# Optimization experiments

Hardware: AMD Instinct MI355X
Metric: run time of the kernel (lower is better)

The kernel has to match this reference:

```python
import jax, jax.numpy as jnp
import numpy as np

BOUND = 1.0 - 1e-16  # margin = 1e-16 (note: rounds to 1.0 in float32, same as torch float32)


def _lpc_to_par(a):
    # Backward Levinson-Durbin: LPC (K, a_1..a_M) -> PARCOR (K, k_1..k_M)
    K, c = a[..., :1], a[..., 1:]
    M = c.shape[-1]
    idx = jnp.arange(M)

    def step(c, m):  # m goes M, M-1, ..., 1
        k = jnp.take(c, m - 1, axis=-1)  # k_m = a_m^(m), shape (B,)
        # paired[j] = a_{m-1-j}^(m) for j=0..m-2 (i.e. a_{m-i} for i=1..m-1)
        paired = jnp.roll(jnp.flip(c, -1), -(M - m + 1), axis=-1)
        c2 = (c - k[..., None] * paired) / (1.0 - k[..., None] ** 2)
        c = jnp.where(idx < m - 1, c2, c)
        return c, k

    _, ks = jax.lax.scan(step, c, jnp.arange(M, 0, -1))
    k1 = jnp.flip(jnp.moveaxis(ks, 0, -1), -1)  # reorder to k_1..k_M, shape (B, M)
    return jnp.concatenate([K, k1], axis=-1)


def _par_to_lpc(k):
    # Forward Levinson-Durbin: PARCOR (K, k_1..k_M) -> LPC (K, a_1..a_M)
    K, kk = k[..., :1], k[..., 1:]
    M = kk.shape[-1]
    idx = jnp.arange(M)
    c0 = jnp.zeros_like(kk)

    def step(c, mk):  # m goes 1..M
        m, km = mk
        paired = jnp.roll(jnp.flip(c, -1), -(M - m + 1), axis=-1)
        c2 = c + km[..., None] * paired
        c = jnp.where(idx < m - 1, c2, c)
        c = jnp.where(idx == m - 1, km[..., None], c)
        return c, None

    ks = jnp.moveaxis(kk, -1, 0)  # (M, B)
    cM, _ = jax.lax.scan(step, c0, (jnp.arange(1, M + 1), ks))
    return jnp.concatenate([K, cM], axis=-1)


def setup_inputs() -> dict:
    key = jax.random.key(0)
    B, M = 2_000_000, 24
    # scale down so the backward Levinson recursion is well-conditioned
    a = 0.05 * jax.random.normal(key, (B, M + 1), dtype=jnp.float32)
    return {"a": a}


def reference(a):
    k = _lpc_to_par(a)
    K, k1 = k[..., :1], k[..., 1:]
    # warn_type='ignore': no side effect; just clip to stability bound
    k1 = jnp.clip(k1, -BOUND, BOUND)
    k2 = jnp.concatenate([K, k1], axis=-1)
    return _par_to_lpc(k2)
```

## Files before the change

### kernel.cpp

```cpp
#include <hip/hip_runtime.h>

#define MM 24
#define ROW_LEN (MM + 1)
#define RPB 256
#define FPB (RPB * ROW_LEN)
#define V4PB (FPB / 4)

__global__ __launch_bounds__(RPB)
void lpc_stab_kernel(const float* __restrict__ a, float* __restrict__ out, int B) {
    __shared__ float lds[FPB];

    const long long total4 = ((long long)B * ROW_LEN) >> 2;
    const long long base4  = (long long)blockIdx.x * V4PB;
    const float4* a4 = (const float4*)a;
    float4*       o4 = (float4*)out;
    float4*       l4 = (float4*)lds;

    #pragma unroll
    for (int it = 0; it < 7; ++it) {
        int li = it * RPB + threadIdx.x;
        if (li < V4PB) {
            long long g = base4 + li;
            if (g < total4) l4[li] = a4[g];
        }
    }
    __syncthreads();

    const int row = blockIdx.x * RPB + threadIdx.x;
    if (row < B) {
        float* p = lds + threadIdx.x * ROW_LEN;
        float K = p[0];
        float c[MM], k[MM];
        #pragma unroll
        for (int j = 0; j < MM; ++j) c[j] = p[j + 1];

        #pragma unroll
        for (int m = MM; m >= 1; --m) {
            float km = c[m - 1];
            k[m - 1] = km;
            if (m >= 2) {
                float inv = __builtin_amdgcn_rcpf(1.0f - km * km);
                #pragma unroll
                for (int i = 0; i < (m - 1) / 2; ++i) {
                    float x = c[i], y = c[m - 2 - i];
                    c[i]         = (x - km * y) * inv;
                    c[m - 2 - i] = (y - km * x) * inv;
                }
                if ((m - 1) & 1) {
                    int i = (m - 1) / 2;
                    float x = c[i];
                    c[i] = (x - km * x) * inv;
                }
            }
        }

        #pragma unroll
        for (int j = 0; j < MM; ++j) k[j] = fminf(fmaxf(k[j], -1.0f), 1.0f);

        #pragma unroll
        for (int m = 1; m <= MM; ++m) {
            float km = k[m - 1];
            #pragma unroll
            for (int i = 0; i < (m - 1) / 2; ++i) {
                float x = c[i], y = c[m - 2 - i];
                c[i]         = x + km * y;
                c[m - 2 - i] = y + km * x;
            }
            if ((m >= 2) && ((m - 1) & 1)) {
                int i = (m - 1) / 2;
                c[i] = c[i] + km * c[i];
            }
            c[m - 1] = km;
        }

        p[0] = K;
        #pragma unroll
        for (int j = 0; j < MM; ++j) p[j + 1] = c[j];
    }
    __syncthreads();

    #pragma unroll
    for (int it = 0; it < 7; ++it) {
        int li = it * RPB + threadIdx.x;
        if (li < V4PB) {
            long long g = base4 + li;
            if (g < total4) o4[g] = l4[li];
        }
    }
}

extern "C" void kernel_launch(void* const* d_in, const int* in_sizes, int n_in,
                              void* d_out, int out_size, void* d_ws, size_t ws_size,
                              hipStream_t stream) {
    const float* a = (const float*)d_in[0];
    float* out = (float*)d_out;
    int B = in_sizes[0] / ROW_LEN;
    int blocks = (B + RPB - 1) / RPB;
    lpc_stab_kernel<<<blocks, RPB, 0, stream>>>(a, out, B);
}
```

Measured before the change: 332.4 us.

## Drop LDS staging, load rows directly into registers and fuse the clip

Each thread now reads its own 25-float row straight from global memory with float4 loads into registers, instead of staging the block's rows through shared memory with barriers. The clip is folded into the backward recursion, overwriting the coefficient in place, so the separate k array is gone. The launch bound now asks for 8 blocks per CU. This is meant to remove the LDS footprint, the two barriers and the extra register array to raise occupancy. In exchange, global accesses are strided per thread and the float4 loads are misaligned on most rows, since rows are 100 bytes apart.

Result: slower. 507.8 us (+52.8%).

```diff
diff --git a/kernel.cpp b/kernel.cpp
--- a/kernel.cpp
+++ b/kernel.cpp
@@ -1,92 +1,64 @@
 #include <hip/hip_runtime.h>
 
 #define MM 24
-#define ROW_LEN (MM + 1)
-#define RPB 256
-#define FPB (RPB * ROW_LEN)
-#define V4PB (FPB / 4)
+#define ROW_LEN 25
+#define TPB 256
 
-__global__ __launch_bounds__(RPB)
+__global__ __launch_bounds__(TPB, 8)
 void lpc_stab_kernel(const float* __restrict__ a, float* __restrict__ out, int B) {
-    __shared__ float lds[FPB];
+    const long long row = (long long)blockIdx.x * TPB + threadIdx.x;
+    if (row >= B) return;
+    const float* gi = a + row * ROW_LEN;
+    float*       go = out + row * ROW_LEN;
 
-    const long long total4 = ((long long)B * ROW_LEN) >> 2;
-    const long long base4  = (long long)blockIdx.x * V4PB;
-    const float4* a4 = (const float4*)a;
-    float4*       o4 = (float4*)out;
-    float4*       l4 = (float4*)lds;
+    float c[ROW_LEN];
+
+    c[24] = gi[24];
+    #pragma unroll
+    for (int i = 5; i >= 0; --i)
+        *(float4*)(c + 4 * i) = *(const float4*)(gi + 4 * i);
+
+    float* cc = c + 1;
 
     #pragma unroll
-    for (int it = 0; it < 7; ++it) {
-        int li = it * RPB + threadIdx.x;
-        if (li < V4PB) {
-            long long g = base4 + li;
-            if (g < total4) l4[li] = a4[g];
+    for (int m = MM; m >= 1; --m) {
+        const float km = cc[m - 1];
+        cc[m - 1] = fminf(fmaxf(km, -1.0f), 1.0f);
+        if (m >= 2) {
+            const float inv = __builtin_amdgcn_rcpf(1.0f - km * km);
+            #pragma unroll
+            for (int i = 0; i < (m - 1) / 2; ++i) {
+                const float x = cc[i], y = cc[m - 2 - i];
+                cc[i]         = (x - km * y) * inv;
+                cc[m - 2 - i] = (y - km * x) * inv;
+            }
+            if ((m - 1) & 1) {
+                const int i = (m - 1) / 2;
+                const float x = cc[i];
+                cc[i] = (x - km * x) * inv;
+            }
         }
     }
-    __syncthreads();
-
-    const int row = blockIdx.x * RPB + threadIdx.x;
-    if (row < B) {
-        float* p = lds + threadIdx.x * ROW_LEN;
-        float K = p[0];
-        float c[MM], k[MM];
-        #pragma unroll
-        for (int j = 0; j < MM; ++j) c[j] = p[j + 1];
-
-        #pragma unroll
-        for (int m = MM; m >= 1; --m) {
-            float km = c[m - 1];
-            k[m - 1] = km;
-            if (m >= 2) {
-                float inv = __builtin_amdgcn_rcpf(1.0f - km * km);
-                #pragma unroll
-                for (int i = 0; i < (m - 1) / 2; ++i) {
-                    float x = c[i], y = c[m - 2 - i];
-                    c[i]         = (x - km * y) * inv;
-                    c[m - 2 - i] = (y - km * x) * inv;
-                }
-                if ((m - 1) & 1) {
-                    int i = (m - 1) / 2;
-                    float x = c[i];
-                    c[i] = (x - km * x) * inv;
-                }
-            }
-        }
-
-        #pragma unroll
-        for (int j = 0; j < MM; ++j) k[j] = fminf(fmaxf(k[j], -1.0f), 1.0f);
-
-        #pragma unroll
-        for (int m = 1; m <= MM; ++m) {
-            float km = k[m - 1];
-            #pragma unroll
-            for (int i = 0; i < (m - 1) / 2; ++i) {
-                float x = c[i], y = c[m - 2 - i];
-                c[i]         = x + km * y;
-                c[m - 2 - i] = y + km * x;
-            }
-            if ((m >= 2) && ((m - 1) & 1)) {
-                int i = (m - 1) / 2;
-                c[i] = c[i] + km * c[i];
-            }
-            c[m - 1] = km;
-        }
-
-        p[0] = K;
-        #pragma unroll
-        for (int j = 0; j < MM; ++j) p[j + 1] = c[j];
-    }
-    __syncthreads();
 
     #pragma unroll
-    for (int it = 0; it < 7; ++it) {
-        int li = it * RPB + threadIdx.x;
-        if (li < V4PB) {
-            long long g = base4 + li;
-            if (g < total4) o4[g] = l4[li];
+    for (int m = 1; m <= MM; ++m) {
+        const float km = cc[m - 1];
+        #pragma unroll
+        for (int i = 0; i < (m - 1) / 2; ++i) {
+            const float x = cc[i], y = cc[m - 2 - i];
+            cc[i]         = x + km * y;
+            cc[m - 2 - i] = y + km * x;
+        }
+        if ((m >= 2) && ((m - 1) & 1)) {
+            const int i = (m - 1) / 2;
+            cc[i] = cc[i] + km * cc[i];
         }
     }
+
+    #pragma unroll
+    for (int i = 0; i < 6; ++i)
+        *(float4*)(go + 4 * i) = *(const float4*)(c + 4 * i);
+    go[24] = c[24];
 }
 
 extern "C" void kernel_launch(void* const* d_in, const int* in_sizes, int n_in,
@@ -95,6 +67,6 @@
     const float* a = (const float*)d_in[0];
     float* out = (float*)d_out;
     int B = in_sizes[0] / ROW_LEN;
-    int blocks = (B + RPB - 1) / RPB;
-    lpc_stab_kernel<<<blocks, RPB, 0, stream>>>(a, out, B);
+    int blocks = (B + TPB - 1) / TPB;
+    lpc_stab_kernel<<<blocks, TPB, 0, stream>>>(a, out, B);
 }
```
